# Kernel tuning notes

Hardware: AMD Instinct MI355X
Metric: run time of the kernel (lower is better)

The kernel has to match this reference:

```python
import jax, jax.numpy as jnp
import numpy as np


def setup_inputs() -> dict:
    key = jax.random.key(0)
    kH, kU, kW = jax.random.split(key, 3)
    T, J, D2 = 16384, 1024, 512  # T x 2d context, J x 2d query
    H = jax.random.normal(kH, (T, D2), dtype=jnp.float32)
    U = jax.random.normal(kU, (J, D2), dtype=jnp.float32)
    Ws = jax.random.normal(kW, (3 * D2, 1), dtype=jnp.float32) * 0.05
    return {"H": H, "U": U, "Ws": Ws}


def reference(H, U, Ws):
    D2 = H.shape[-1]
    # Ws applied to concat([H_dup, U_dup, H_dup*U_dup]) decomposes into three blocks.
    w1 = Ws[:D2, 0]          # (2d,)
    w2 = Ws[D2:2 * D2, 0]    # (2d,)
    w3 = Ws[2 * D2:, 0]      # (2d,)
    # Trilinear similarity S[t, j] = H[t]@w1 + U[j]@w2 + (H[t]*U[j])@w3  -> (T, J)
    S = (H @ w1)[:, None] + (U @ w2)[None, :] + (H * w3) @ U.T
    # C2Q attention: softmax over query axis, attend query vectors -> (T, 2d)
    attended_query = jax.nn.softmax(S, axis=-1) @ U
    # Q2C attention: softmax over T of max_j S, rank-1 summary of context -> (2d,)
    b = jax.nn.softmax(jnp.max(S, axis=-1))
    h_tilde = b @ H  # (2d,), tiled to (T, 2d) by broadcasting
    # Merge to query-aware representation G -> (T, 8d)
    G = jnp.concatenate(
        [H, attended_query, H * attended_query, H * h_tilde[None, :]], axis=-1
    )
    return G
```

## Files before the change

kernel.cpp:

```cpp
#include <hip/hip_runtime.h>
#include <hip/hip_bf16.h>

#define T_ROWS 16384
#define J_DIM  1024
#define D_DIM  512

typedef __attribute__((ext_vector_type(8))) short bf16x8;
typedef __attribute__((ext_vector_type(4))) float f32x4;
typedef unsigned short u16;

__device__ __forceinline__ u16 f2bf(float f) {
    union { float f; unsigned int u; } v; v.f = f;
    return (u16)((v.u + 0x7FFFu + ((v.u >> 16) & 1u)) >> 16);
}
__device__ __forceinline__ float bf2f(u16 b) {
    union { unsigned int u; float f; } v; v.u = ((unsigned int)b) << 16;
    return v.f;
}

__device__ __forceinline__ void gload16(const void* g, void* l) {
    __builtin_amdgcn_global_load_lds(
        (__attribute__((address_space(1))) void*)(unsigned long long)(size_t)g,
        (__attribute__((address_space(3))) void*)(unsigned int)(size_t)l,
        16, 0, 0);
}

template<int NT>
__device__ __forceinline__ void gemm_core(
    const u16* A, int lda, const u16* B, int ldb, u16* lds, f32x4 (&acc)[4][4])
{
    const int tid  = threadIdx.x;
    const int lane = tid & 63;
    const int w    = tid >> 6;
    const int wr   = w >> 1, wc = w & 1;
    const int fr   = lane & 15, quad = lane >> 4;

    const int srow = tid >> 2;
    const int ss   = (tid & 3) ^ ((srow >> 1) & 3);

    const u16* gA0 = A + (size_t)srow * lda + ss * 8;
    const u16* gA1 = A + (size_t)(srow + 64) * lda + ss * 8;
    const u16* gB0 = B + (size_t)srow * ldb + ss * 8;
    const u16* gB1 = B + (size_t)(srow + 64) * ldb + ss * 8;

    u16* As = lds;
    u16* Bs = lds + 8192;
    u16* dA0 = As + tid * 8;
    u16* dA1 = As + 2048 + tid * 8;
    u16* dB0 = Bs + tid * 8;
    u16* dB1 = Bs + 2048 + tid * 8;

    gload16(gA0, dA0); gload16(gA1, dA1);
    gload16(gB0, dB0); gload16(gB1, dB1);
    gA0 += 32; gA1 += 32; gB0 += 32; gB1 += 32;

    int offA[4], offB[4];
    #pragma unroll
    for (int i = 0; i < 4; ++i) {
        const int rA = wr * 64 + i * 16 + fr;
        offA[i] = rA * 32 + (quad ^ ((rA >> 1) & 3)) * 8;
        const int rB = wc * 64 + i * 16 + fr;
        offB[i] = rB * 32 + (quad ^ ((rB >> 1) & 3)) * 8;
    }
    __syncthreads();

    #pragma unroll 2
    for (int t = 0; t < NT; ++t) {
        const int cur = (t & 1) * 4096;
        const int nxt = 4096 - cur;
        if (t + 1 < NT) {
            gload16(gA0, dA0 + nxt); gload16(gA1, dA1 + nxt);
            gload16(gB0, dB0 + nxt); gload16(gB1, dB1 + nxt);
            gA0 += 32; gA1 += 32; gB0 += 32; gB1 += 32;
        }
        const u16* Ac = As + cur;
        const u16* Bc = Bs + cur;
        bf16x8 af[4], bfr[4];
        #pragma unroll
        for (int i = 0; i < 4; ++i) af[i]  = *(const bf16x8*)(Ac + offA[i]);
        #pragma unroll
        for (int i = 0; i < 4; ++i) bfr[i] = *(const bf16x8*)(Bc + offB[i]);
        #pragma unroll
        for (int mf = 0; mf < 4; ++mf)
            #pragma unroll
            for (int nf = 0; nf < 4; ++nf)
                acc[mf][nf] = __builtin_amdgcn_mfma_f32_16x16x32_bf16(
                    af[mf], bfr[nf], acc[mf][nf], 0, 0, 0);
        __syncthreads();
    }
}

__global__ __launch_bounds__(256) void prep_kernel(
    const float* __restrict__ H, const float* __restrict__ U,
    const float* __restrict__ Ws,
    float* __restrict__ hw1, float* __restrict__ uw2,
    u16* outU, u16* __restrict__ Ub, u16* __restrict__ Utp)
{
    const int w = threadIdx.x >> 6, lane = threadIdx.x & 63;
    if (blockIdx.x < 4096) {
        const int i = blockIdx.x * 4 + w;
        const float* hp = H + (size_t)i * D_DIM + lane * 8;
        const float4 a = *(const float4*)hp;
        const float4 b = *(const float4*)(hp + 4);
        const float4 w1a = *(const float4*)(Ws + lane * 8);
        const float4 w1b = *(const float4*)(Ws + lane * 8 + 4);
        const float4 w3a = *(const float4*)(Ws + 2 * D_DIM + lane * 8);
        const float4 w3b = *(const float4*)(Ws + 2 * D_DIM + lane * 8 + 4);
        float p = a.x*w1a.x + a.y*w1a.y + a.z*w1a.z + a.w*w1a.w
                + b.x*w1b.x + b.y*w1b.y + b.z*w1b.z + b.w*w1b.w;
        #pragma unroll
        for (int m = 1; m < 64; m <<= 1) p += __shfl_xor(p, m);
        if (lane == 0) hw1[i] = p;
        bf16x8 q;
        q[0] = (short)f2bf(a.x * w3a.x); q[1] = (short)f2bf(a.y * w3a.y);
        q[2] = (short)f2bf(a.z * w3a.z); q[3] = (short)f2bf(a.w * w3a.w);
        q[4] = (short)f2bf(b.x * w3b.x); q[5] = (short)f2bf(b.y * w3b.y);
        q[6] = (short)f2bf(b.z * w3b.z); q[7] = (short)f2bf(b.w * w3b.w);
        *(bf16x8*)(outU + (size_t)i * 4096 + 3072 + lane * 8) = q;
    } else {
        const int j = (blockIdx.x - 4096) * 4 + w;
        const float* up = U + (size_t)j * D_DIM + lane * 8;
        const float4 a = *(const float4*)up;
        const float4 b = *(const float4*)(up + 4);
        const float4 w2a = *(const float4*)(Ws + D_DIM + lane * 8);
        const float4 w2b = *(const float4*)(Ws + D_DIM + lane * 8 + 4);
        float p = a.x*w2a.x + a.y*w2a.y + a.z*w2a.z + a.w*w2a.w
                + b.x*w2b.x + b.y*w2b.y + b.z*w2b.z + b.w*w2b.w;
        #pragma unroll
        for (int m = 1; m < 64; m <<= 1) p += __shfl_xor(p, m);
        if (lane == 0) uw2[j] = p;
        bf16x8 q;
        q[0] = (short)f2bf(a.x); q[1] = (short)f2bf(a.y);
        q[2] = (short)f2bf(a.z); q[3] = (short)f2bf(a.w);
        q[4] = (short)f2bf(b.x); q[5] = (short)f2bf(b.y);
        q[6] = (short)f2bf(b.z); q[7] = (short)f2bf(b.w);
        *(bf16x8*)(Ub + (size_t)j * D_DIM + lane * 8) = q;
        const size_t jpart = (size_t)(j >> 5) * 512
                           + (size_t)(((j >> 3) & 3) * 128) + (j & 7);
        #pragma unroll
        for (int s = 0; s < 8; ++s) {
            const int d = lane * 8 + s;
            Utp[(size_t)(d >> 4) * 16384 + jpart + (size_t)(d & 15) * 8] = (u16)q[s];
        }
    }
}

__global__ __launch_bounds__(256) void s_gemm(
    u16* outU, const u16* __restrict__ Ub, const float* __restrict__ uw2,
    float* __restrict__ pmax)
{
    __shared__ u16 lds[16896];
    __shared__ float redf[256];
    const int bid = blockIdx.x;
    const int swz = (bid & 7) * 128 + (bid >> 3);
    const int bm = swz >> 3, nb = swz & 7;

    f32x4 acc[4][4];
    #pragma unroll
    for (int i = 0; i < 4; ++i)
        #pragma unroll
        for (int j = 0; j < 4; ++j) acc[i][j] = (f32x4){0.f, 0.f, 0.f, 0.f};

    gemm_core<16>(outU + (size_t)bm * 128 * 4096 + 3072, 4096,
                  Ub + (size_t)nb * 128 * 512, 512, lds, acc);

    const int tid = threadIdx.x, lane = tid & 63, w = tid >> 6;
    const int wr = w >> 1, wc = w & 1, fr = lane & 15, quad = lane >> 4;
    float u2[4];
    #pragma unroll
    for (int nf = 0; nf < 4; ++nf) u2[nf] = uw2[nb * 128 + wc * 64 + nf * 16 + fr];

    u16* Tl = lds;
    #pragma unroll
    for (int mf = 0; mf < 4; ++mf)
        #pragma unroll
        for (int m = 0; m < 4; ++m) {
            const int row = wr * 64 + mf * 16 + quad * 4 + m;
            float mv = -1e30f;
            #pragma unroll
            for (int nf = 0; nf < 4; ++nf) {
                acc[mf][nf][m] += u2[nf];
                mv = fmaxf(mv, acc[mf][nf][m]);
            }
            mv = fmaxf(mv, __shfl_xor(mv, 1));
            mv = fmaxf(mv, __shfl_xor(mv, 2));
            mv = fmaxf(mv, __shfl_xor(mv, 4));
            mv = fmaxf(mv, __shfl_xor(mv, 8));
            if (fr == 0) redf[wc * 128 + row] = mv;
            #pragma unroll
            for (int nf = 0; nf < 4; ++nf)
                Tl[row * 132 + wc * 64 + nf * 16 + fr] = f2bf(acc[mf][nf][m]);
        }
    __syncthreads();

    if (wc == 0 && fr == 0) {
        #pragma unroll
        for (int mf = 0; mf < 4; ++mf)
            #pragma unroll
            for (int m = 0; m < 4; ++m) {
                const int rr = wr * 64 + mf * 16 + quad * 4 + m;
                pmax[((size_t)bm * 128 + rr) * 8 + nb] =
                    fmaxf(redf[rr], redf[128 + rr]);
            }
    }

    {
        const int rr = tid >> 1, hf = tid & 1;
        const u16* src = Tl + rr * 132 + hf * 64;
        u16* dst = outU + (size_t)(bm * 128 + rr) * 4096 + 1024 + nb * 128 + hf * 64;
        #pragma unroll
        for (int i = 0; i < 8; ++i)
            *(bf16x8*)(dst + i * 8) = *(const bf16x8*)(src + i * 8);
    }
}

__global__ __launch_bounds__(1024) void bsoft2(
    const float* __restrict__ pmax, const float* __restrict__ hw1,
    float* __restrict__ bvec)
{
    __shared__ float red[16];
    __shared__ float Msh, Lsh;
    const int t = threadIdx.x;
    float rs[16];
    #pragma unroll
    for (int e = 0; e < 16; ++e) {
        const int r = t + e * 1024;
        const float4 p0 = *(const float4*)(pmax + (size_t)r * 8);
        const float4 p1 = *(const float4*)(pmax + (size_t)r * 8 + 4);
        rs[e] = fmaxf(fmaxf(fmaxf(p0.x, p0.y), fmaxf(p0.z, p0.w)),
                      fmaxf(fmaxf(p1.x, p1.y), fmaxf(p1.z, p1.w))) + hw1[r];
    }
    float m = -1e30f;
    #pragma unroll
    for (int e = 0; e < 16; ++e) m = fmaxf(m, rs[e]);
    #pragma unroll
    for (int s = 1; s < 64; s <<= 1) m = fmaxf(m, __shfl_xor(m, s));
    if ((t & 63) == 0) red[t >> 6] = m;
    __syncthreads();
    if (t == 0) {
        float M = red[0];
        for (int i = 1; i < 16; ++i) M = fmaxf(M, red[i]);
        Msh = M;
    }
    __syncthreads();
    const float M = Msh;
    float l = 0.f;
    #pragma unroll
    for (int e = 0; e < 16; ++e) l += __expf(rs[e] - M);
    #pragma unroll
    for (int s = 1; s < 64; s <<= 1) l += __shfl_xor(l, s);
    if ((t & 63) == 0) red[t >> 6] = l;
    __syncthreads();
    if (t == 0) {
        float L = 0.f;
        for (int i = 0; i < 16; ++i) L += red[i];
        Lsh = L;
    }
    __syncthreads();
    const float invL = 1.f / Lsh;
    #pragma unroll
    for (int e = 0; e < 16; ++e) bvec[t + e * 1024] = __expf(rs[e] - M) * invL;
}

__global__ __launch_bounds__(512) void htilde_partial(
    const float* __restrict__ H, const float* __restrict__ b,
    float* __restrict__ part)
{
    const int blk = blockIdx.x;
    const int d = threadIdx.x;
    const int i0 = blk * 64;
    float s = 0.f;
    for (int rI = 0; rI < 64; ++rI)
        s += b[i0 + rI] * H[(size_t)(i0 + rI) * D_DIM + d];
    part[(size_t)blk * D_DIM + d] = s;
}

__global__ __launch_bounds__(512) void htilde_reduce(
    const float* __restrict__ part, float* __restrict__ ht)
{
    const int d = threadIdx.x;
    float s = 0.f;
    for (int p = 0; p < 256; ++p) s += part[(size_t)p * D_DIM + d];
    ht[d] = s;
}

__global__ __launch_bounds__(512, 4) void pv_fused(
    u16* outU, const u16* __restrict__ Utp, const float* __restrict__ H,
    const float* __restrict__ htld)
{
    __shared__ float SPf[32 * 520];
    u16* SP = (u16*)SPf;
    const int tid = threadIdx.x, lane = tid & 63, w = tid >> 6;
    const int fr = lane & 15, quad = lane >> 4;
    const int ib = blockIdx.x * 32;

    #pragma unroll
    for (int p = 0; p < 8; ++p) {
        const int slot = p * 512 + tid;
        const int r  = slot >> 7;
        const int c8 = slot & 127;
        gload16(outU + (size_t)(ib + r) * 4096 + 1024 + (size_t)((c8 ^ (r & 7)) * 8),
                SP + (size_t)slot * 8);
    }
    __syncthreads();

    #pragma unroll
    for (int rr = 0; rr < 4; ++rr) {
        const int r = w * 4 + rr;
        u16* row = SP + (size_t)r * 1024;
        const int s0 = (lane ^ (r & 7)) * 8;
        const int s1 = ((lane + 64) ^ (r & 7)) * 8;
        bf16x8 x0 = *(bf16x8*)(row + s0);
        bf16x8 x1 = *(bf16x8*)(row + s1);
        float f0[8], f1[8];
        float mx = -1e30f;
        #pragma unroll
        for (int i = 0; i < 8; ++i) {
            f0[i] = bf2f((u16)x0[i]); f1[i] = bf2f((u16)x1[i]);
            mx = fmaxf(mx, fmaxf(f0[i], f1[i]));
        }
        #pragma unroll
        for (int s = 1; s < 64; s <<= 1) mx = fmaxf(mx, __shfl_xor(mx, s));
        float sum = 0.f;
        #pragma unroll
        for (int i = 0; i < 8; ++i) {
            f0[i] = __expf(f0[i] - mx); f1[i] = __expf(f1[i] - mx);
            sum += f0[i] + f1[i];
        }
        #pragma unroll
        for (int s = 1; s < 64; s <<= 1) sum += __shfl_xor(sum, s);
        const float inv = 1.f / sum;
        bf16x8 y0, y1;
        #pragma unroll
        for (int i = 0; i < 8; ++i) {
            y0[i] = (short)f2bf(f0[i] * inv);
            y1[i] = (short)f2bf(f1[i] * inv);
        }
        *(bf16x8*)(row + s0) = y0;
        *(bf16x8*)(row + s1) = y1;
    }
    __syncthreads();

    f32x4 acc[2][4];
    #pragma unroll
    for (int i = 0; i < 2; ++i)
        #pragma unroll
        for (int j = 0; j < 4; ++j) acc[i][j] = (f32x4){0.f, 0.f, 0.f, 0.f};

    const u16* bp = Utp + (size_t)lane * 8;
    bf16x8 bA[4], bB[4];
    #pragma unroll
    for (int nf = 0; nf < 4; ++nf)
        bA[nf] = *(const bf16x8*)(bp + ((size_t)(w * 4 + nf) * 32) * 512);

    for (int ks = 0; ks < 32; ks += 2) {
        #pragma unroll
        for (int nf = 0; nf < 4; ++nf)
            bB[nf] = *(const bf16x8*)(bp + ((size_t)(w * 4 + nf) * 32 + ks + 1) * 512);
        bf16x8 a0[2];
        #pragma unroll
        for (int mf = 0; mf < 2; ++mf)
            a0[mf] = *(const bf16x8*)(SP + (size_t)(mf * 16 + fr) * 1024
                                         + (size_t)(((ks * 4 + quad) ^ (fr & 7)) * 8));
        __builtin_amdgcn_s_setprio(1);
        #pragma unroll
        for (int mf = 0; mf < 2; ++mf)
            #pragma unroll
            for (int nf = 0; nf < 4; ++nf)
                acc[mf][nf] = __builtin_amdgcn_mfma_f32_16x16x32_bf16(
                    a0[mf], bA[nf], acc[mf][nf], 0, 0, 0);
        __builtin_amdgcn_s_setprio(0);
        if (ks + 2 < 32) {
            #pragma unroll
            for (int nf = 0; nf < 4; ++nf)
                bA[nf] = *(const bf16x8*)(bp + ((size_t)(w * 4 + nf) * 32 + ks + 2) * 512);
        }
        bf16x8 a1[2];
        #pragma unroll
        for (int mf = 0; mf < 2; ++mf)
            a1[mf] = *(const bf16x8*)(SP + (size_t)(mf * 16 + fr) * 1024
                                         + (size_t)((((ks + 1) * 4 + quad) ^ (fr & 7)) * 8));
        __builtin_amdgcn_s_setprio(1);
        #pragma unroll
        for (int mf = 0; mf < 2; ++mf)
            #pragma unroll
            for (int nf = 0; nf < 4; ++nf)
                acc[mf][nf] = __builtin_amdgcn_mfma_f32_16x16x32_bf16(
                    a1[mf], bB[nf], acc[mf][nf], 0, 0, 0);
        __builtin_amdgcn_s_setprio(0);
    }
    __syncthreads();

    #pragma unroll
    for (int mf = 0; mf < 2; ++mf)
        #pragma unroll
        for (int m = 0; m < 4; ++m) {
            const int r = mf * 16 + quad * 4 + m;
            #pragma unroll
            for (int nf = 0; nf < 4; ++nf)
                SPf[r * 520 + w * 64 + nf * 16 + fr] = acc[mf][nf][m];
        }
    __syncthreads();

    {
        const int r = tid >> 4;
        const int l16 = tid & 15;
        const size_t grow = (size_t)ib + r;
        const float* hrow = H + grow * D_DIM;
        float* ob = (float*)outU + grow * 2048;
        #pragma unroll
        for (int i = 0; i < 8; ++i) {
            const int c = l16 * 4 + i * 64;
            const float4 h  = *(const float4*)(hrow + c);
            const float4 aq = *(const float4*)(&SPf[r * 520 + c]);
            const float4 hv = *(const float4*)(htld + c);
            float4 ha, hh;
            ha.x = h.x * aq.x; ha.y = h.y * aq.y; ha.z = h.z * aq.z; ha.w = h.w * aq.w;
            hh.x = h.x * hv.x; hh.y = h.y * hv.y; hh.z = h.z * hv.z; hh.w = h.w * hv.w;
            *(float4*)(ob + c)        = h;
            *(float4*)(ob + 512 + c)  = aq;
            *(float4*)(ob + 1024 + c) = ha;
            *(float4*)(ob + 1536 + c) = hh;
        }
    }
}

extern "C" void kernel_launch(void* const* d_in, const int* in_sizes, int n_in,
                              void* d_out, int out_size, void* d_ws, size_t ws_size,
                              hipStream_t stream)
{
    const float* H  = (const float*)d_in[0];
    const float* U  = (const float*)d_in[1];
    const float* Ws = (const float*)d_in[2];
    u16* outU = (u16*)d_out;

    float* uw2   = (float*)d_ws;
    float* hw1   = uw2 + 1024;
    float* bvec  = hw1 + T_ROWS;
    float* htld  = bvec + T_ROWS;
    float* part  = htld + D_DIM;
    float* pmax  = part + 256 * D_DIM;
    u16*   Ub    = (u16*)(pmax + (size_t)T_ROWS * 8);
    u16*   Utp   = Ub + (size_t)J_DIM * D_DIM;

    hipLaunchKernelGGL(prep_kernel, dim3(4096 + 256), dim3(256), 0, stream,
                       H, U, Ws, hw1, uw2, outU, Ub, Utp);
    hipLaunchKernelGGL(s_gemm, dim3(1024), dim3(256), 0, stream,
                       outU, Ub, uw2, pmax);
    hipLaunchKernelGGL(bsoft2, dim3(1), dim3(1024), 0, stream, pmax, hw1, bvec);
    hipLaunchKernelGGL(htilde_partial, dim3(256), dim3(512), 0, stream, H, bvec, part);
    hipLaunchKernelGGL(htilde_reduce, dim3(1), dim3(512), 0, stream, part, htld);
    hipLaunchKernelGGL(pv_fused, dim3(T_ROWS / 32), dim3(512), 0, stream,
                       outU, Utp, H, htld);
}
```

Baseline: 135.9 us.

## Fuse Q2C softmax and h_tilde reduction into one cooperative grid kernel

Replaces the single-block softmax kernel and the two h_tilde kernels with one cooperative kernel of 256 blocks. Grid-wide syncs handle the global max and sum reductions, and each block folds its unnormalized exponentials directly into a partial weighted sum of H. This removes two kernel launches and the serial 1-block softmax over 16K rows. In exchange it adds three grid.sync barriers, leaves the final reduce on a single block, and depends on cooperative launch support.

```diff
diff --git a/kernel.cpp b/kernel.cpp
--- a/kernel.cpp
+++ b/kernel.cpp
@@ -1,5 +1,8 @@
 #include <hip/hip_runtime.h>
 #include <hip/hip_bf16.h>
+#include <hip/hip_cooperative_groups.h>
+
+namespace cg = cooperative_groups;
 
 #define T_ROWS 16384
 #define J_DIM  1024
@@ -214,74 +217,93 @@
     }
 }
 
-__global__ __launch_bounds__(1024) void bsoft2(
+__global__ __launch_bounds__(512) void stats_coop(
     const float* __restrict__ pmax, const float* __restrict__ hw1,
-    float* __restrict__ bvec)
-{
-    __shared__ float red[16];
+    const float* __restrict__ H,
+    float* __restrict__ partM, float* __restrict__ partL,
+    float* __restrict__ part, float* __restrict__ htld)
+{
+    cg::grid_group grid = cg::this_grid();
+    const int b = blockIdx.x;
+    const int t = threadIdx.x;
+    __shared__ float rssh[64];
+    __shared__ float esh[64];
+    __shared__ float red8[8];
     __shared__ float Msh, Lsh;
-    const int t = threadIdx.x;
-    float rs[16];
-    #pragma unroll
-    for (int e = 0; e < 16; ++e) {
-        const int r = t + e * 1024;
-        const float4 p0 = *(const float4*)(pmax + (size_t)r * 8);
-        const float4 p1 = *(const float4*)(pmax + (size_t)r * 8 + 4);
-        rs[e] = fmaxf(fmaxf(fmaxf(p0.x, p0.y), fmaxf(p0.z, p0.w)),
-                      fmaxf(fmaxf(p1.x, p1.y), fmaxf(p1.z, p1.w))) + hw1[r];
-    }
-    float m = -1e30f;
-    #pragma unroll
-    for (int e = 0; e < 16; ++e) m = fmaxf(m, rs[e]);
-    #pragma unroll
-    for (int s = 1; s < 64; s <<= 1) m = fmaxf(m, __shfl_xor(m, s));
-    if ((t & 63) == 0) red[t >> 6] = m;
-    __syncthreads();
-    if (t == 0) {
-        float M = red[0];
-        for (int i = 1; i < 16; ++i) M = fmaxf(M, red[i]);
-        Msh = M;
-    }
-    __syncthreads();
-    const float M = Msh;
-    float l = 0.f;
-    #pragma unroll
-    for (int e = 0; e < 16; ++e) l += __expf(rs[e] - M);
-    #pragma unroll
-    for (int s = 1; s < 64; s <<= 1) l += __shfl_xor(l, s);
-    if ((t & 63) == 0) red[t >> 6] = l;
-    __syncthreads();
-    if (t == 0) {
-        float L = 0.f;
-        for (int i = 0; i < 16; ++i) L += red[i];
-        Lsh = L;
-    }
-    __syncthreads();
-    const float invL = 1.f / Lsh;
-    #pragma unroll
-    for (int e = 0; e < 16; ++e) bvec[t + e * 1024] = __expf(rs[e] - M) * invL;
-}
-
-__global__ __launch_bounds__(512) void htilde_partial(
-    const float* __restrict__ H, const float* __restrict__ b,
-    float* __restrict__ part)
-{
-    const int blk = blockIdx.x;
-    const int d = threadIdx.x;
-    const int i0 = blk * 64;
-    float s = 0.f;
-    for (int rI = 0; rI < 64; ++rI)
-        s += b[i0 + rI] * H[(size_t)(i0 + rI) * D_DIM + d];
-    part[(size_t)blk * D_DIM + d] = s;
-}
-
-__global__ __launch_bounds__(512) void htilde_reduce(
-    const float* __restrict__ part, float* __restrict__ ht)
-{
-    const int d = threadIdx.x;
-    float s = 0.f;
-    for (int p = 0; p < 256; ++p) s += part[(size_t)p * D_DIM + d];
-    ht[d] = s;
+
+    {
+        const int r = b * 64 + (t >> 3);
+        float v = pmax[(size_t)b * 512 + t];
+        v = fmaxf(v, __shfl_xor(v, 1));
+        v = fmaxf(v, __shfl_xor(v, 2));
+        v = fmaxf(v, __shfl_xor(v, 4));
+        const float rs = v + hw1[r];
+        if ((t & 7) == 0) rssh[t >> 3] = rs;
+        float bm = rs;
+        bm = fmaxf(bm, __shfl_xor(bm, 8));
+        bm = fmaxf(bm, __shfl_xor(bm, 16));
+        bm = fmaxf(bm, __shfl_xor(bm, 32));
+        if ((t & 63) == 0) red8[t >> 6] = bm;
+        __syncthreads();
+        if (t == 0) {
+            float M = red8[0];
+            #pragma unroll
+            for (int i = 1; i < 8; ++i) M = fmaxf(M, red8[i]);
+            partM[b] = M;
+        }
+    }
+    grid.sync();
+    {
+        float m = (t < 256) ? partM[t] : -1e30f;
+        #pragma unroll
+        for (int s = 1; s < 64; s <<= 1) m = fmaxf(m, __shfl_xor(m, s));
+        if ((t & 63) == 0) red8[t >> 6] = m;
+        __syncthreads();
+        if (t == 0) {
+            float M = red8[0];
+            #pragma unroll
+            for (int i = 1; i < 8; ++i) M = fmaxf(M, red8[i]);
+            Msh = M;
+        }
+        __syncthreads();
+        const float M = Msh;
+        if (t < 64) esh[t] = __expf(rssh[t] - M);
+        __syncthreads();
+        if (t == 0) {
+            float l = 0.f;
+            #pragma unroll 8
+            for (int i = 0; i < 64; ++i) l += esh[i];
+            partL[b] = l;
+        }
+    }
+    grid.sync();
+    {
+        float l = (t < 256) ? partL[t] : 0.f;
+        #pragma unroll
+        for (int s = 1; s < 64; s <<= 1) l += __shfl_xor(l, s);
+        if ((t & 63) == 0) red8[t >> 6] = l;
+        __syncthreads();
+        if (t == 0) {
+            float L = 0.f;
+            #pragma unroll
+            for (int i = 0; i < 8; ++i) L += red8[i];
+            Lsh = L;
+        }
+        __syncthreads();
+        const float invL = 1.f / Lsh;
+        float s = 0.f;
+        const float* hp = H + (size_t)b * 64 * D_DIM + t;
+        #pragma unroll 8
+        for (int ri = 0; ri < 64; ++ri)
+            s += esh[ri] * hp[(size_t)ri * D_DIM];
+        part[(size_t)b * D_DIM + t] = s * invL;
+    }
+    grid.sync();
+    if (b == 0) {
+        float s = 0.f;
+        for (int p = 0; p < 256; ++p) s += part[(size_t)p * D_DIM + t];
+        htld[t] = s;
+    }
 }
 
 __global__ __launch_bounds__(512, 4) void pv_fused(
@@ -436,9 +458,10 @@
 
     float* uw2   = (float*)d_ws;
     float* hw1   = uw2 + 1024;
-    float* bvec  = hw1 + T_ROWS;
-    float* htld  = bvec + T_ROWS;
-    float* part  = htld + D_DIM;
+    float* htld  = hw1 + T_ROWS;
+    float* partM = htld + D_DIM;
+    float* partL = partM + 256;
+    float* part  = partL + 256;
     float* pmax  = part + 256 * D_DIM;
     u16*   Ub    = (u16*)(pmax + (size_t)T_ROWS * 8);
     u16*   Utp   = Ub + (size_t)J_DIM * D_DIM;
@@ -447,9 +470,15 @@
                        H, U, Ws, hw1, uw2, outU, Ub, Utp);
     hipLaunchKernelGGL(s_gemm, dim3(1024), dim3(256), 0, stream,
                        outU, Ub, uw2, pmax);
-    hipLaunchKernelGGL(bsoft2, dim3(1), dim3(1024), 0, stream, pmax, hw1, bvec);
-    hipLaunchKernelGGL(htilde_partial, dim3(256), dim3(512), 0, stream, H, bvec, part);
-    hipLaunchKernelGGL(htilde_reduce, dim3(1), dim3(512), 0, stream, part, htld);
+    {
+        const float* pmax_c = pmax;
+        const float* hw1_c  = hw1;
+        const float* H_c    = H;
+        void* cargs[] = { (void*)&pmax_c, (void*)&hw1_c, (void*)&H_c,
+                          (void*)&partM, (void*)&partL, (void*)&part, (void*)&htld };
+        hipLaunchCooperativeKernel((const void*)stats_coop, dim3(256), dim3(512),
+                                   cargs, 0, stream);
+    }
     hipLaunchKernelGGL(pv_fused, dim3(T_ROWS / 32), dim3(512), 0, stream,
                        outU, Utp, H, htld);
 }
```

Result: slower. 213.1 us (+56.8%).
